# Performance work log

Hardware: AMD Instinct MI355X
Metric: run time of the kernel (lower is better)

The kernel has to match this reference:

```python
import jax, jax.numpy as jnp
import numpy as np

N = 50000        # nodes
E = 800000       # directed edges
NUM_E = 10000    # hyperedges
NFEAT, NHID, NOUT = 256, 128, 64
K = 10
TEMP = 5.0


def gcn_prop(h, src, dst, n):
    # PyG GCNConv propagation with added self-loops: D^-1/2 (A+I) D^-1/2 h
    ew = jnp.ones(src.shape[0], h.dtype)
    deg = 1.0 + jax.ops.segment_sum(ew, dst, num_segments=n)  # self-loop adds 1
    dinv = jax.lax.rsqrt(deg)
    norm = dinv[src] * dinv[dst]                   # [E]
    out = jax.ops.segment_sum(h[src] * norm[:, None], dst, num_segments=n)
    out = out + h / deg[:, None]                   # self-loop term (weight deg^-1)
    return out


def gcn_conv(x, W, b, src, dst, n):
    return gcn_prop(x @ W, src, dst, n) + b


def hgnnp_conv(x, W, b, hv, he, n, num_e):
    # dhg HGNNPConv: theta(x) then v->e mean aggregation, then e->v mean
    h = x @ W + b
    ones = jnp.ones(hv.shape[0], h.dtype)
    e_deg = jnp.maximum(jax.ops.segment_sum(ones, he, num_segments=num_e), 1.0)
    v_deg = jnp.maximum(jax.ops.segment_sum(ones, hv, num_segments=n), 1.0)
    e_feat = jax.ops.segment_sum(h[hv], he, num_segments=num_e) / e_deg[:, None]
    v_out = jax.ops.segment_sum(e_feat[he], hv, num_segments=n) / v_deg[:, None]
    return v_out


def setup_inputs() -> dict:
    key = jax.random.key(0)
    ks = jax.random.split(key, 12)
    x = jax.random.normal(ks[0], (N, NFEAT), jnp.float32)
    edge_index = jax.random.randint(ks[1], (2, E), 0, N)
    hv_idx = jax.random.randint(ks[2], (200000,), 0, N)
    he_idx = jax.random.randint(ks[3], (200000,), 0, NUM_E)

    def glorot(k, shape):
        lim = float(np.sqrt(6.0 / (shape[0] + shape[1])))
        return jax.random.uniform(k, shape, jnp.float32, -lim, lim)

    return {
        "x": x, "edge_index": edge_index, "hv_idx": hv_idx, "he_idx": he_idx,
        "gcn_W1": glorot(ks[4], (NFEAT, NHID)), "gcn_b1": jnp.zeros((NHID,), jnp.float32),
        "gcn_W2": glorot(ks[5], (NHID, NOUT)), "gcn_b2": jnp.zeros((NOUT,), jnp.float32),
        "hg_W1": glorot(ks[6], (NFEAT, NHID)), "hg_b1": jnp.zeros((NHID,), jnp.float32),
        "hg_W2": glorot(ks[7], (NHID, NOUT)), "hg_b2": jnp.zeros((NOUT,), jnp.float32),
        "num_iter": 1,
    }


def reference(x, edge_index, hv_idx, he_idx,
              gcn_W1, gcn_b1, gcn_W2, gcn_b2,
              hg_W1, hg_b1, hg_W2, hg_b2, num_iter):
    src, dst = edge_index[0], edge_index[1]

    # HGNNP_GCN encoder (dropout is identity in eval-style reference)
    x1 = jax.nn.relu(gcn_conv(x, gcn_W1, gcn_b1, src, dst, N))
    x2 = gcn_conv(x1, gcn_W2, gcn_b2, src, dst, N)
    x3 = jax.nn.relu(hgnnp_conv(x, hg_W1, hg_b1, hv_idx, he_idx, N, NUM_E))
    x4 = hgnnp_conv(x3, hg_W2, hg_b2, hv_idx, he_idx, N, NUM_E)  # is_last: no act
    embeds = x2 * 0.5 + x4 * 0.5                     # [N, NOUT]

    # row-normalize (diag(1/||row||) @ data)
    data = embeds / jnp.linalg.norm(embeds, axis=1, keepdims=True)

    # kmeans++ init is a host-side, data-dependent pick; use deterministic
    # strided row selection from the (detached) normalized embeddings.
    init_idx = jnp.arange(K) * (N // K)
    mu = jax.lax.stop_gradient(data[init_idx])       # [K, NOUT]

    for _ in range(int(num_iter)):
        dist = data @ mu.T                           # [N, K]
        r = jax.nn.softmax(TEMP * dist, axis=1)
        cluster_r = r.sum(axis=0)                    # [K]
        cluster_mean = r.T @ data                    # [K, NOUT]
        mu = cluster_mean / cluster_r[:, None]

    dist = data @ mu.T
    r = jax.nn.softmax(TEMP * dist, axis=1)
    return mu, r, embeds, dist
```

## Files before the change

### kernel.cpp

```cpp
#include <hip/hip_runtime.h>
#include <hip/hip_bf16.h>


#define NN   50000
#define NP   50048
#define EE   800000
#define NINC 200000
#define NEH  10000
#define KCL  10

#define MU_OFF  0
#define R_OFF   640
#define EMB_OFF 500640
#define D_OFF   3700640

typedef __hip_bfloat16 bf16;
typedef unsigned short u16;
typedef unsigned int   u32;
typedef __attribute__((ext_vector_type(8))) short short8;
typedef __attribute__((ext_vector_type(4))) float f32x4;

__device__ __forceinline__ float b2f(bf16 v){ return __bfloat162float(v); }
__device__ __forceinline__ float us2f(u16 u){ return __uint_as_float(((unsigned)u) << 16); }
__device__ __forceinline__ u16 f2bu(float f){
  unsigned u = __float_as_uint(f);
  return (u16)((u + 0x7fffu + ((u >> 16) & 1u)) >> 16);
}
__device__ __forceinline__ bf16 f2b(float f){
  u16 r = f2bu(f);
  bf16 h;
  reinterpret_cast<u16&>(h) = r;
  return h;
}
__device__ __forceinline__ float ldf(const void* p, size_t i, int isbf){
  return isbf ? b2f(((const bf16*)p)[i]) : ((const float*)p)[i];
}
__device__ __forceinline__ void stf(void* p, size_t i, float v, int isbf){
  if (isbf) ((bf16*)p)[i] = f2b(v);
  else      ((float*)p)[i] = v;
}

__global__ void k_detect(const u16* __restrict__ xr, int* flag){
  __shared__ int bad;
  if (threadIdx.x == 0) bad = 0;
  __syncthreads();
  for (int i = threadIdx.x; i < 4096; i += 256){
    int e = (xr[i] >> 7) & 0xFF;
    if (e >= 0xEF) bad = 1;
  }
  __syncthreads();
  if (threadIdx.x == 0) *flag = bad ? 0 : 1;
}

__global__ void k_aconv(const void* __restrict__ x, u16* __restrict__ xb,
                        const int* __restrict__ flag){
  int i = blockIdx.x*256 + threadIdx.x;
  const int n4 = NN*256/4;
  if (i >= n4) return;
  ushort4 o;
  if (flag[0]){
    o = ((const ushort4*)x)[i];
  } else {
    float4 v = ((const float4*)x)[i];
    o = make_ushort4(f2bu(v.x), f2bu(v.y), f2bu(v.z), f2bu(v.w));
  }
  ((ushort4*)xb)[i] = o;
}

__global__ void k_wprep(const void* gW1, const void* hW1, const void* gW2, const void* hW2,
                        const void* gb1, const void* hb1, const void* gb2, const void* hb2,
                        u16* gW1t, u16* hW1t, u16* gW2t, u16* hW2t,
                        float* gb1f, float* hb1f, float* gb2f, float* hb2f,
                        const int* __restrict__ flag){
  const int isbf = flag[0];
  int i = blockIdx.x*256 + threadIdx.x;
  if (i < 256*128){
    int n = i >> 8, k = i & 255;
    gW1t[i] = f2bu(ldf(gW1, (size_t)k*128 + n, isbf));
    hW1t[i] = f2bu(ldf(hW1, (size_t)k*128 + n, isbf));
  }
  if (i < 64*128){
    int n = i >> 7, k = i & 127;
    gW2t[i] = f2bu(ldf(gW2, (size_t)k*64 + n, isbf));
    hW2t[i] = f2bu(ldf(hW2, (size_t)k*64 + n, isbf));
  }
  if (i < 128){ gb1f[i] = ldf(gb1,i,isbf); hb1f[i] = ldf(hb1,i,isbf); }
  if (i < 64) { gb2f[i] = ldf(gb2,i,isbf); hb2f[i] = ldf(hb2,i,isbf); }
}

template<int NBKT, int NPB>
__global__ __launch_bounds__(256) void k_histA(const int* __restrict__ key,
                                               int* __restrict__ HA, int chunk){
  __shared__ u32 hist[NBKT];
  for (int i = threadIdx.x; i < NBKT; i += 256) hist[i] = 0;
  __syncthreads();
  int base = blockIdx.x*chunk;
  for (int i = threadIdx.x; i < chunk; i += 256)
    atomicAdd(&hist[key[base+i]/NPB], 1u);
  __syncthreads();
  int* out = HA + blockIdx.x*NBKT;
  for (int i = threadIdx.x; i < NBKT; i += 256) out[i] = (int)hist[i];
}

__global__ void k_scanA_all(int* HAg, int* HAv, int* HAe,
                            int* bsg, int* bsv, int* bse){
  int* HA; int* bs; int nch;
  if (blockIdx.x == 0){ HA = HAg; bs = bsg; nch = 128; }
  else if (blockIdx.x == 1){ HA = HAv; bs = bsv; nch = 64; }
  else { HA = HAe; bs = bse; nch = 64; }
  __shared__ int s[256];
  int t = threadIdx.x;
  int run = 0;
  if (t < 250){
    for (int c = 0; c < nch; ++c){
      int v = HA[c*250 + t];
      HA[c*250 + t] = run;
      run += v;
    }
  }
  int own = (t < 250) ? run : 0;
  s[t] = own; __syncthreads();
  #pragma unroll
  for (int off = 1; off < 256; off <<= 1){
    int add = (t >= off) ? s[t-off] : 0;
    __syncthreads();
    s[t] += add;
    __syncthreads();
  }
  if (t < 250) bs[t] = s[t] - own;
  if (t == 255) bs[250] = s[255];
}

template<int NBKT, int NPB>
__global__ __launch_bounds__(256) void k_fillA(const int* __restrict__ key,
    const int* __restrict__ val, const int* __restrict__ HA,
    const int* __restrict__ bs, u32* __restrict__ packed, int chunk){
  __shared__ u32 cur[NBKT];
  const int* pre = HA + blockIdx.x*NBKT;
  for (int i = threadIdx.x; i < NBKT; i += 256) cur[i] = (u32)(bs[i] + pre[i]);
  __syncthreads();
  int base = blockIdx.x*chunk;
  for (int i = threadIdx.x; i < chunk; i += 256){
    int k = key[base+i];
    int b = k / NPB;
    u32 pos = atomicAdd(&cur[b], 1u);
    packed[pos] = ((u32)(k - b*NPB) << 16) | (u32)val[base+i];
  }
}

template<int NPB>
__global__ __launch_bounds__(256) void k_fillB(const u32* __restrict__ packed,
    const int* __restrict__ bs, int* __restrict__ csr,
    int* __restrict__ cnt, int* __restrict__ rp){
  __shared__ u32 hist[NPB];
  __shared__ int s[256];
  __shared__ u32 cur[NPB];
  const int b = blockIdx.x;
  const int s0 = bs[b], m = bs[b+1] - s0;
  const int t = threadIdx.x;
  for (int i = t; i < NPB; i += 256) hist[i] = 0;
  __syncthreads();
  for (int i = t; i < m; i += 256)
    atomicAdd(&hist[packed[s0+i] >> 16], 1u);
  __syncthreads();
  int own = (t < NPB) ? (int)hist[t] : 0;
  s[t] = own; __syncthreads();
  #pragma unroll
  for (int off = 1; off < 256; off <<= 1){
    int add = (t >= off) ? s[t-off] : 0;
    __syncthreads();
    s[t] += add;
    __syncthreads();
  }
  if (t < NPB){
    int excl = s[t] - own;
    cnt[b*NPB + t] = own;
    rp[b*NPB + t]  = s0 + excl;
    cur[t] = (u32)(s0 + excl);
  }
  __syncthreads();
  for (int i = t; i < m; i += 256){
    u32 p = packed[s0+i];
    u32 pos = atomicAdd(&cur[p >> 16], 1u);
    csr[pos] = (int)(p & 0xffffu);
  }
}

__global__ void k_invs(const int* __restrict__ cg, const int* __restrict__ cv,
                       const int* __restrict__ ce,
                       float* dinv, float* invv, float* inve){
  int i = blockIdx.x*256 + threadIdx.x;
  if (i < NN){
    float d = 1.0f + (float)cg[i];
    dinv[i] = rsqrtf(d);
    invv[i] = 1.0f / fmaxf((float)cv[i], 1.0f);
  } else if (i < NP){
    dinv[i] = 0.f;
  }
  if (i < NEH) inve[i] = 1.0f / fmaxf((float)ce[i], 1.0f);
}

template<int KDIM, int NCOL>
__global__ __launch_bounds__(256) void k_gemm_mfma(
    const u16* __restrict__ A, const u16* __restrict__ Wt,
    const float* __restrict__ bias, const float* __restrict__ rowscale,
    u16* __restrict__ C, int relu)
{
  constexpr int NT  = NCOL/16;
  constexpr int LDA = 40;
  __shared__ __align__(16) u16 Asl[64][LDA];
  __shared__ __align__(16) u16 Wsl[NCOL][LDA];
  const int tid  = threadIdx.x;
  const int wave = tid >> 6, lane = tid & 63;
  const int l15 = lane & 15, l4 = lane >> 4;
  const int row0 = blockIdx.x * 64;
  const int ar = tid >> 2, aq = tid & 3;
  constexpr int NW = NCOL*4/256;

  f32x4 acc[NT] = {};

  for (int kk = 0; kk < KDIM; kk += 32){
    {
      uint4 v = *(const uint4*)(A + (size_t)(row0 + ar)*KDIM + kk + aq*8);
      *(uint4*)&Asl[ar][aq*8] = v;
    }
    #pragma unroll
    for (int w2 = 0; w2 < NW; ++w2){
      int c = tid + w2*256;
      int n = c >> 2, q = c & 3;
      uint4 v = *(const uint4*)(Wt + (size_t)n*KDIM + kk + q*8);
      *(uint4*)&Wsl[n][q*8] = v;
    }
    __syncthreads();
    short8 af = *(const short8*)&Asl[wave*16 + l15][l4*8];
    #pragma unroll
    for (int t = 0; t < NT; ++t){
      short8 bf = *(const short8*)&Wsl[t*16 + l15][l4*8];
      acc[t] = __builtin_amdgcn_mfma_f32_16x16x32_bf16(af, bf, acc[t], 0, 0, 0);
    }
    __syncthreads();
  }

  #pragma unroll
  for (int t = 0; t < NT; ++t){
    int gcol = t*16 + l15;
    float b = bias ? bias[gcol] : 0.f;
    #pragma unroll
    for (int e = 0; e < 4; ++e){
      int grow = row0 + wave*16 + l4*4 + e;
      float v = acc[t][e] + b;
      if (relu) v = fmaxf(v, 0.f);
      if (rowscale) v *= rowscale[grow];
      C[(size_t)grow*NCOL + gcol] = f2bu(v);
    }
  }
}

template<int F, bool OUTBF, bool SELF>
__global__ __launch_bounds__(256) void k_gather(
    const int* __restrict__ rp, const int* __restrict__ cnt,
    const int* __restrict__ csr, const float* __restrict__ scale,
    const u16* __restrict__ h, const float* __restrict__ bias,
    void* __restrict__ out, int relu)
{
  const int wave = threadIdx.x >> 6, lane = threadIdx.x & 63;
  const int d = blockIdx.x*4 + wave;
  const int k0 = rp[d], n = cnt[d];

  if constexpr (F == 128){
    const uint* h32 = (const uint*)h;
    float a0=0,a1=0,b0=0,b1=0,c0=0,c1=0,e0=0,e1=0;
    if (SELF){
      uint v = h32[(size_t)d*64 + lane];
      a0 = us2f((u16)v); a1 = us2f((u16)(v>>16));
    }
    for (int base = 0; base < n; base += 64){
      int mm = n - base; if (mm > 64) mm = 64;
      int idx = (lane < mm) ? csr[k0 + base + lane] : 0;
      int jj = 0;
      for (; jj + 4 <= mm; jj += 4){
        int s0=__shfl(idx,jj), s1=__shfl(idx,jj+1), s2=__shfl(idx,jj+2), s3=__shfl(idx,jj+3);
        uint v0 = h32[(size_t)s0*64 + lane];
        uint v1 = h32[(size_t)s1*64 + lane];
        uint v2 = h32[(size_t)s2*64 + lane];
        uint v3 = h32[(size_t)s3*64 + lane];
        a0 += us2f((u16)v0); a1 += us2f((u16)(v0>>16));
        b0 += us2f((u16)v1); b1 += us2f((u16)(v1>>16));
        c0 += us2f((u16)v2); c1 += us2f((u16)(v2>>16));
        e0 += us2f((u16)v3); e1 += us2f((u16)(v3>>16));
      }
      for (; jj < mm; ++jj){
        int s = __shfl(idx, jj);
        uint v = h32[(size_t)s*64 + lane];
        a0 += us2f((u16)v); a1 += us2f((u16)(v>>16));
      }
    }
    float sc = scale[d];
    float o0 = ((a0+b0)+(c0+e0))*sc;
    float o1 = ((a1+b1)+(c1+e1))*sc;
    if (bias){ o0 += bias[lane*2]; o1 += bias[lane*2+1]; }
    if (relu){ o0 = fmaxf(o0,0.f); o1 = fmaxf(o1,0.f); }
    if (OUTBF){
      ((uint*)out)[(size_t)d*64 + lane] = (uint)f2bu(o0) | ((uint)f2bu(o1) << 16);
    } else {
      ((float2*)out)[(size_t)d*64 + lane] = make_float2(o0, o1);
    }
  } else {
    float a=0,b=0,c=0,e=0;
    if (SELF) a = us2f(h[(size_t)d*64 + lane]);
    for (int base = 0; base < n; base += 64){
      int mm = n - base; if (mm > 64) mm = 64;
      int idx = (lane < mm) ? csr[k0 + base + lane] : 0;
      int jj = 0;
      for (; jj + 4 <= mm; jj += 4){
        int s0=__shfl(idx,jj), s1=__shfl(idx,jj+1), s2=__shfl(idx,jj+2), s3=__shfl(idx,jj+3);
        a += us2f(h[(size_t)s0*64 + lane]);
        b += us2f(h[(size_t)s1*64 + lane]);
        c += us2f(h[(size_t)s2*64 + lane]);
        e += us2f(h[(size_t)s3*64 + lane]);
      }
      for (; jj < mm; ++jj){
        int s = __shfl(idx, jj);
        a += us2f(h[(size_t)s*64 + lane]);
      }
    }
    float o = ((a+b)+(c+e))*scale[d];
    if (bias) o += bias[lane];
    if (relu) o = fmaxf(o, 0.f);
    if (OUTBF) ((u16*)out)[(size_t)d*64 + lane] = f2bu(o);
    else       ((float*)out)[(size_t)d*64 + lane] = o;
  }
}

__global__ void k_embeds(const float* __restrict__ x2, const float* __restrict__ x4,
                         void* __restrict__ out, float* __restrict__ data,
                         const int* __restrict__ flag){
  int row  = blockIdx.x*4 + (threadIdx.x >> 6);
  int lane = threadIdx.x & 63;
  if (row >= NN) return;
  size_t idx = (size_t)row*64 + lane;
  float v = 0.5f*(x2[idx] + x4[idx]);
  float ss = v*v;
  #pragma unroll
  for (int off=32; off>0; off>>=1) ss += __shfl_xor(ss, off);
  float inv = rsqrtf(ss);
  data[idx] = v*inv;
  stf(out, EMB_OFF + idx, v, flag[0]);
}

__global__ void k_mu_init(const float* __restrict__ data, float* __restrict__ mu){
  int p = blockIdx.x*256 + threadIdx.x;
  if (p >= KCL*64) return;
  int k = p >> 6, f = p & 63;
  mu[p] = data[(size_t)k*(NN/KCL)*64 + f];
}

__global__ __launch_bounds__(640) void k_cluster_iter(const float* __restrict__ data,
    const float* __restrict__ mu, float* __restrict__ part, float* __restrict__ pcr,
    const int* __restrict__ nit, int iter)
{
  if (iter >= nit[0]) return;
  __shared__ float ms[640];
  __shared__ float rl[250][KCL];
  const int tid = threadIdx.x;
  ms[tid] = mu[tid];
  __syncthreads();
  const int r0 = blockIdx.x*250;
  if (tid < 250){
    const float4* dr = (const float4*)(data + (size_t)(r0 + tid)*64);
    float dot[KCL];
    #pragma unroll
    for (int k=0;k<KCL;k++) dot[k]=0.f;
    #pragma unroll
    for (int q=0;q<16;q++){
      float4 v = dr[q];
      #pragma unroll
      for (int k=0;k<KCL;k++){
        float4 m4 = *(const float4*)&ms[k*64+q*4];
        dot[k] = fmaf(v.x,m4.x,fmaf(v.y,m4.y,fmaf(v.z,m4.z,fmaf(v.w,m4.w,dot[k]))));
      }
    }
    float m = -1e30f;
    #pragma unroll
    for (int k=0;k<KCL;k++) m = fmaxf(m, 5.0f*dot[k]);
    float s = 0.f, ev[KCL];
    #pragma unroll
    for (int k=0;k<KCL;k++){ ev[k] = expf(5.0f*dot[k]-m); s += ev[k]; }
    float inv = 1.0f/s;
    #pragma unroll
    for (int k=0;k<KCL;k++) rl[tid][k] = ev[k]*inv;
  }
  __syncthreads();
  const int w = tid >> 6, f = tid & 63;
  float acc = 0.f, crp = 0.f;
  for (int t = 0; t < 250; ++t){
    float rv = rl[t][w];
    acc = fmaf(rv, data[(size_t)(r0+t)*64 + f], acc);
    crp += rv;
  }
  part[(size_t)blockIdx.x*640 + tid] = acc;
  if (f == 0) pcr[blockIdx.x*16 + w] = crp;
}

__global__ void k_creduce(const float* __restrict__ part, const float* __restrict__ pcr,
                          float* __restrict__ csum, float* __restrict__ cr,
                          const int* __restrict__ nit, int iter){
  if (iter >= nit[0]) return;
  int p = threadIdx.x;
  if (p < 640){
    float a = 0.f;
    for (int b = 0; b < 200; ++b) a += part[(size_t)b*640 + p];
    csum[p] = a;
  } else if (p < 640 + KCL){
    int k = p - 640;
    float a = 0.f;
    for (int b = 0; b < 200; ++b) a += pcr[b*16 + k];
    cr[k] = a;
  }
}

__global__ void k_mu_update(float* __restrict__ mu, const float* __restrict__ csum,
                            const float* __restrict__ cr,
                            const int* __restrict__ nit, int iter){
  if (iter >= nit[0]) return;
  int p = threadIdx.x;
  mu[p] = csum[p] / cr[p >> 6];
}

__global__ __launch_bounds__(256) void k_cluster_final(const float* __restrict__ data,
    const float* __restrict__ mu, void* __restrict__ out, const int* __restrict__ flag)
{
  __shared__ float ms[640];
  const int tid = threadIdx.x;
  for (int j = tid; j < 640; j += 256) ms[j] = mu[j];
  __syncthreads();
  int row = blockIdx.x*256 + tid;
  if (row >= NN) return;
  const int isbf = flag[0];
  const float4* dr = (const float4*)(data + (size_t)row*64);
  float dot[KCL];
  #pragma unroll
  for (int k=0;k<KCL;k++) dot[k]=0.f;
  #pragma unroll
  for (int q=0;q<16;q++){
    float4 v = dr[q];
    #pragma unroll
    for (int k=0;k<KCL;k++){
      float4 m4 = *(const float4*)&ms[k*64+q*4];
      dot[k] = fmaf(v.x,m4.x,fmaf(v.y,m4.y,fmaf(v.z,m4.z,fmaf(v.w,m4.w,dot[k]))));
    }
  }
  float m = -1e30f;
  #pragma unroll
  for (int k=0;k<KCL;k++) m = fmaxf(m, 5.0f*dot[k]);
  float s = 0.f, ev[KCL];
  #pragma unroll
  for (int k=0;k<KCL;k++){ ev[k] = expf(5.0f*dot[k]-m); s += ev[k]; }
  float inv = 1.0f/s;
  #pragma unroll
  for (int k=0;k<KCL;k++){
    stf(out, (size_t)D_OFF + (size_t)row*KCL + k, dot[k],    isbf);
    stf(out, (size_t)R_OFF + (size_t)row*KCL + k, ev[k]*inv, isbf);
  }
}

__global__ void k_mu_out(const float* __restrict__ mu, void* __restrict__ out,
                         const int* __restrict__ flag){
  int p = blockIdx.x*256 + threadIdx.x;
  if (p < KCL*64) stf(out, MU_OFF + p, mu[p], flag[0]);
}

extern "C" void kernel_launch(void* const* d_in, const int* in_sizes, int n_in,
                              void* d_out, int out_size, void* d_ws, size_t ws_size,
                              hipStream_t stream)
{
  const void* x   = d_in[0];
  const int*  ei  = (const int*)d_in[1];
  const int*  hv  = (const int*)d_in[2];
  const int*  he  = (const int*)d_in[3];
  const void* gW1 = d_in[4];
  const void* gb1 = d_in[5];
  const void* gW2 = d_in[6];
  const void* gb2 = d_in[7];
  const void* hW1 = d_in[8];
  const void* hb1 = d_in[9];
  const void* hW2 = d_in[10];
  const void* hb2 = d_in[11];
  const int*  nit = (const int*)d_in[12];

  float* ws = (float*)d_ws;
  size_t o = 0;
  u16*   xb  = (u16*)(ws + o); o += (size_t)NP*128;
  u16*   BAb = (u16*)(ws + o); o += (size_t)NP*64;
  u16*   BBb = (u16*)(ws + o); o += (size_t)NP*64;
  u16*   BCb = (u16*)(ws + o); o += (size_t)NP*64;
  u16*   BDb = (u16*)(ws + o); o += (size_t)NEH*64;
  u16*  gW1t = (u16*)(ws + o); o += 16384;
  u16*  hW1t = (u16*)(ws + o); o += 16384;
  u16*  gW2t = (u16*)(ws + o); o += 4096;
  u16*  hW2t = (u16*)(ws + o); o += 4096;
  float* gb1f = ws + o; o += 128;
  float* hb1f = ws + o; o += 128;
  float* gb2f = ws + o; o += 64;
  float* hb2f = ws + o; o += 64;
  float* dinv = ws + o; o += 50048;
  float* invv = ws + o; o += 50048;
  float* inve = ws + o; o += 10048;
  float* mu   = ws + o; o += 640;
  float* csum = ws + o; o += 640;
  float* cr   = ws + o; o += 64;
  float* part = ws + o; o += 200*640;
  float* pcr  = ws + o; o += 200*16;
  int*   dflg = (int*)(ws + o); o += 16;
  float* x2f   = (float*)xb;
  float* x4f   = (float*)xb + (size_t)NP*64;
  float* dataf = (float*)BBb;
  int* ib = (int*)(ws + o);
  size_t io = 0;
  int* cg    = ib + io; io += NN;
  int* cv    = ib + io; io += NN;
  int* ce    = ib + io; io += NEH + 48;
  int* rp_g  = ib + io; io += NN;
  int* rp_v  = ib + io; io += NN;
  int* rp_e  = ib + io; io += NEH + 48;
  int* csr_g = ib + io; io += EE;
  int* csr_e = ib + io; io += NINC;
  int* csr_v = ib + io; io += NINC;
  int* HAg   = ib + io; io += 128*250;
  int* HAv   = ib + io; io += 64*250;
  int* HAe   = ib + io; io += 64*250;
  int* bsg   = ib + io; io += 256;
  int* bsv   = ib + io; io += 256;
  int* bse   = ib + io; io += 256;
  u32* pg = (u32*)(ib + io); io += EE;
  u32* pv = (u32*)(ib + io); io += NINC;
  u32* pe = (u32*)(ib + io); io += NINC;

  const int* srcp = ei;
  const int* dstp = ei + EE;
  dim3 B(256);
  const int NBP = (NP + 255)/256;

  k_detect<<<dim3(1), B, 0, stream>>>((const u16*)x, dflg);
  k_aconv<<<dim3(12500), B, 0, stream>>>(x, xb, dflg);
  k_wprep<<<dim3(128), B, 0, stream>>>(gW1, hW1, gW2, hW2, gb1, hb1, gb2, hb2,
                                       gW1t, hW1t, gW2t, hW2t,
                                       gb1f, hb1f, gb2f, hb2f, dflg);

  k_histA<250,200><<<dim3(128), B, 0, stream>>>(dstp, HAg, 6250);
  k_histA<250,200><<<dim3(64),  B, 0, stream>>>(hv,   HAv, 3125);
  k_histA<250, 40><<<dim3(64),  B, 0, stream>>>(he,   HAe, 3125);
  k_scanA_all<<<dim3(3), B, 0, stream>>>(HAg, HAv, HAe, bsg, bsv, bse);
  k_fillA<250,200><<<dim3(128), B, 0, stream>>>(dstp, srcp, HAg, bsg, pg, 6250);
  k_fillA<250,200><<<dim3(64),  B, 0, stream>>>(hv,   he,   HAv, bsv, pv, 3125);
  k_fillA<250, 40><<<dim3(64),  B, 0, stream>>>(he,   hv,   HAe, bse, pe, 3125);
  k_fillB<200><<<dim3(250), B, 0, stream>>>(pg, bsg, csr_g, cg, rp_g);
  k_fillB<200><<<dim3(250), B, 0, stream>>>(pv, bsv, csr_v, cv, rp_v);
  k_fillB< 40><<<dim3(250), B, 0, stream>>>(pe, bse, csr_e, ce, rp_e);
  k_invs<<<dim3(NBP), B, 0, stream>>>(cg, cv, ce, dinv, invv, inve);

  const int NB = NP/64;
  k_gemm_mfma<256,128><<<dim3(NB), B, 0, stream>>>(xb, gW1t, nullptr, dinv, BAb, 0);
  k_gather<128,true,true><<<dim3(NN/4), B, 0, stream>>>(rp_g, cg, csr_g, dinv,
                                                        BAb, gb1f, BBb, 1);
  k_gemm_mfma<256,128><<<dim3(NB), B, 0, stream>>>(xb, hW1t, hb1f, nullptr, BAb, 0);
  k_gather<128,true,false><<<dim3(NEH/4), B, 0, stream>>>(rp_e, ce, csr_e, inve,
                                                          BAb, nullptr, BDb, 0);
  k_gather<128,true,false><<<dim3(NN/4), B, 0, stream>>>(rp_v, cv, csr_v, invv,
                                                         BDb, nullptr, BCb, 1);
  k_gemm_mfma<128,64><<<dim3(NB), B, 0, stream>>>(BBb, gW2t, nullptr, dinv, BAb, 0);
  k_gather<64,false,true><<<dim3(NN/4), B, 0, stream>>>(rp_g, cg, csr_g, dinv,
                                                        BAb, gb2f, x2f, 0);
  k_gemm_mfma<128,64><<<dim3(NB), B, 0, stream>>>(BCb, hW2t, hb2f, nullptr, BAb, 0);
  k_gather<64,true,false><<<dim3(NEH/4), B, 0, stream>>>(rp_e, ce, csr_e, inve,
                                                         BAb, nullptr, BDb, 0);
  k_gather<64,false,false><<<dim3(NN/4), B, 0, stream>>>(rp_v, cv, csr_v, invv,
                                                         BDb, nullptr, x4f, 0);

  k_embeds<<<dim3((NN+3)/4), B, 0, stream>>>(x2f, x4f, d_out, dataf, dflg);

  k_mu_init<<<dim3(3), B, 0, stream>>>(dataf, mu);
  for (int it = 0; it < 4; ++it){
    k_cluster_iter<<<dim3(200), dim3(640), 0, stream>>>(dataf, mu, part, pcr, nit, it);
    k_creduce     <<<dim3(1),   dim3(768), 0, stream>>>(part, pcr, csum, cr, nit, it);
    k_mu_update   <<<dim3(1),   dim3(640), 0, stream>>>(mu, csum, cr, nit, it);
  }
  k_cluster_final<<<dim3(196), B, 0, stream>>>(dataf, mu, d_out, dflg);
  k_mu_out       <<<dim3(3),  B, 0, stream>>>(mu, d_out, dflg);
}
```

Measured before the change: 380.5 us.

## Retile k-means cluster kernels into 64-row smem tiles with two-stage reduction

The cluster iteration and final kernels now process 64 rows per block across 782 blocks, staging the data tile in padded shared memory. All 640 threads compute row-by-cluster dot products, where previously only 250 threads did the full work. The single-block reduction of block partials is split into a 40-block first stage and a small second stage to handle the larger partial count. This aims to raise parallelism in the clustering phase, at the cost of an extra launch per iteration and more partial-sum traffic.

```diff
diff --git a/kernel.cpp b/kernel.cpp
--- a/kernel.cpp
+++ b/kernel.cpp
@@ -8,6 +8,7 @@
 #define NINC 200000
 #define NEH  10000
 #define KCL  10
+#define CBLK 782
 
 #define MU_OFF  0
 #define R_OFF   640
@@ -361,60 +362,88 @@
 {
   if (iter >= nit[0]) return;
   __shared__ float ms[640];
-  __shared__ float rl[250][KCL];
+  __shared__ float dt[64][65];
+  __shared__ float ds[64][11];
   const int tid = threadIdx.x;
   ms[tid] = mu[tid];
-  __syncthreads();
-  const int r0 = blockIdx.x*250;
-  if (tid < 250){
-    const float4* dr = (const float4*)(data + (size_t)(r0 + tid)*64);
+  const int base = blockIdx.x*64;
+  for (int i = tid; i < 4096; i += 640){
+    int r = i >> 6, f = i & 63;
+    int grow = base + r;
+    dt[r][f] = (grow < NN) ? data[(size_t)grow*64 + f] : 0.f;
+  }
+  __syncthreads();
+  {
+    const int row = tid & 63, k = tid >> 6;
+    float dot = 0.f;
+    #pragma unroll 16
+    for (int f = 0; f < 64; ++f)
+      dot = fmaf(dt[row][f], ms[k*64 + f], dot);
+    ds[row][k] = dot;
+  }
+  __syncthreads();
+  if (tid < 64){
     float dot[KCL];
     #pragma unroll
-    for (int k=0;k<KCL;k++) dot[k]=0.f;
-    #pragma unroll
-    for (int q=0;q<16;q++){
-      float4 v = dr[q];
-      #pragma unroll
-      for (int k=0;k<KCL;k++){
-        float4 m4 = *(const float4*)&ms[k*64+q*4];
-        dot[k] = fmaf(v.x,m4.x,fmaf(v.y,m4.y,fmaf(v.z,m4.z,fmaf(v.w,m4.w,dot[k]))));
-      }
-    }
+    for (int k = 0; k < KCL; ++k) dot[k] = ds[tid][k];
     float m = -1e30f;
     #pragma unroll
-    for (int k=0;k<KCL;k++) m = fmaxf(m, 5.0f*dot[k]);
+    for (int k = 0; k < KCL; ++k) m = fmaxf(m, 5.0f*dot[k]);
     float s = 0.f, ev[KCL];
     #pragma unroll
-    for (int k=0;k<KCL;k++){ ev[k] = expf(5.0f*dot[k]-m); s += ev[k]; }
-    float inv = 1.0f/s;
-    #pragma unroll
-    for (int k=0;k<KCL;k++) rl[tid][k] = ev[k]*inv;
-  }
-  __syncthreads();
-  const int w = tid >> 6, f = tid & 63;
-  float acc = 0.f, crp = 0.f;
-  for (int t = 0; t < 250; ++t){
-    float rv = rl[t][w];
-    acc = fmaf(rv, data[(size_t)(r0+t)*64 + f], acc);
-    crp += rv;
-  }
-  part[(size_t)blockIdx.x*640 + tid] = acc;
-  if (f == 0) pcr[blockIdx.x*16 + w] = crp;
-}
-
-__global__ void k_creduce(const float* __restrict__ part, const float* __restrict__ pcr,
-                          float* __restrict__ csum, float* __restrict__ cr,
-                          const int* __restrict__ nit, int iter){
+    for (int k = 0; k < KCL; ++k){ ev[k] = expf(5.0f*dot[k]-m); s += ev[k]; }
+    float inv = (base + tid < NN) ? 1.0f/s : 0.f;
+    #pragma unroll
+    for (int k = 0; k < KCL; ++k) ds[tid][k] = ev[k]*inv;
+  }
+  __syncthreads();
+  {
+    const int f = tid & 63, k = tid >> 6;
+    float acc = 0.f, crp = 0.f;
+    #pragma unroll 8
+    for (int t = 0; t < 64; ++t){
+      float rv = ds[t][k];
+      acc = fmaf(rv, dt[t][f], acc);
+      crp += rv;
+    }
+    part[(size_t)blockIdx.x*640 + tid] = acc;
+    if (f == 0) pcr[blockIdx.x*16 + k] = crp;
+  }
+}
+
+__global__ void k_cred1(const float* __restrict__ part, const float* __restrict__ pcr,
+                        float* __restrict__ p2, float* __restrict__ pc2,
+                        const int* __restrict__ nit, int iter){
   if (iter >= nit[0]) return;
-  int p = threadIdx.x;
-  if (p < 640){
+  int b = blockIdx.x, t = threadIdx.x;
+  int r0 = b*20, r1 = r0 + 20; if (r1 > CBLK) r1 = CBLK;
+  if (t < 640){
     float a = 0.f;
-    for (int b = 0; b < 200; ++b) a += part[(size_t)b*640 + p];
-    csum[p] = a;
-  } else if (p < 640 + KCL){
-    int k = p - 640;
+    for (int r = r0; r < r1; ++r) a += part[(size_t)r*640 + t];
+    p2[(size_t)b*640 + t] = a;
+  } else if (t < 640 + KCL){
+    int k = t - 640;
     float a = 0.f;
-    for (int b = 0; b < 200; ++b) a += pcr[b*16 + k];
+    for (int r = r0; r < r1; ++r) a += pcr[r*16 + k];
+    pc2[b*16 + k] = a;
+  }
+}
+
+__global__ void k_cred2(const float* __restrict__ p2, const float* __restrict__ pc2,
+                        float* __restrict__ csum, float* __restrict__ cr,
+                        const int* __restrict__ nit, int iter){
+  if (iter >= nit[0]) return;
+  int t = threadIdx.x;
+  if (t < 640){
+    float a = 0.f;
+    #pragma unroll
+    for (int b = 0; b < 40; ++b) a += p2[(size_t)b*640 + t];
+    csum[t] = a;
+  } else if (t < 640 + KCL){
+    int k = t - 640;
+    float a = 0.f;
+    #pragma unroll
+    for (int b = 0; b < 40; ++b) a += pc2[b*16 + k];
     cr[k] = a;
   }
 }
@@ -427,40 +456,48 @@
   mu[p] = csum[p] / cr[p >> 6];
 }
 
-__global__ __launch_bounds__(256) void k_cluster_final(const float* __restrict__ data,
+__global__ __launch_bounds__(640) void k_cluster_final(const float* __restrict__ data,
     const float* __restrict__ mu, void* __restrict__ out, const int* __restrict__ flag)
 {
   __shared__ float ms[640];
+  __shared__ float dt[64][65];
+  __shared__ float ds[64][11];
   const int tid = threadIdx.x;
-  for (int j = tid; j < 640; j += 256) ms[j] = mu[j];
-  __syncthreads();
-  int row = blockIdx.x*256 + tid;
-  if (row >= NN) return;
-  const int isbf = flag[0];
-  const float4* dr = (const float4*)(data + (size_t)row*64);
-  float dot[KCL];
-  #pragma unroll
-  for (int k=0;k<KCL;k++) dot[k]=0.f;
-  #pragma unroll
-  for (int q=0;q<16;q++){
-    float4 v = dr[q];
-    #pragma unroll
-    for (int k=0;k<KCL;k++){
-      float4 m4 = *(const float4*)&ms[k*64+q*4];
-      dot[k] = fmaf(v.x,m4.x,fmaf(v.y,m4.y,fmaf(v.z,m4.z,fmaf(v.w,m4.w,dot[k]))));
-    }
-  }
-  float m = -1e30f;
-  #pragma unroll
-  for (int k=0;k<KCL;k++) m = fmaxf(m, 5.0f*dot[k]);
-  float s = 0.f, ev[KCL];
-  #pragma unroll
-  for (int k=0;k<KCL;k++){ ev[k] = expf(5.0f*dot[k]-m); s += ev[k]; }
-  float inv = 1.0f/s;
-  #pragma unroll
-  for (int k=0;k<KCL;k++){
-    stf(out, (size_t)D_OFF + (size_t)row*KCL + k, dot[k],    isbf);
-    stf(out, (size_t)R_OFF + (size_t)row*KCL + k, ev[k]*inv, isbf);
+  ms[tid] = mu[tid];
+  const int base = blockIdx.x*64;
+  for (int i = tid; i < 4096; i += 640){
+    int r = i >> 6, f = i & 63;
+    int grow = base + r;
+    dt[r][f] = (grow < NN) ? data[(size_t)grow*64 + f] : 0.f;
+  }
+  __syncthreads();
+  {
+    const int row = tid & 63, k = tid >> 6;
+    float dot = 0.f;
+    #pragma unroll 16
+    for (int f = 0; f < 64; ++f)
+      dot = fmaf(dt[row][f], ms[k*64 + f], dot);
+    ds[row][k] = dot;
+  }
+  __syncthreads();
+  if (tid < 64 && base + tid < NN){
+    const int row = base + tid;
+    const int isbf = flag[0];
+    float dot[KCL];
+    #pragma unroll
+    for (int k = 0; k < KCL; ++k) dot[k] = ds[tid][k];
+    float m = -1e30f;
+    #pragma unroll
+    for (int k = 0; k < KCL; ++k) m = fmaxf(m, 5.0f*dot[k]);
+    float s = 0.f, ev[KCL];
+    #pragma unroll
+    for (int k = 0; k < KCL; ++k){ ev[k] = expf(5.0f*dot[k]-m); s += ev[k]; }
+    float inv = 1.0f/s;
+    #pragma unroll
+    for (int k = 0; k < KCL; ++k){
+      stf(out, (size_t)D_OFF + (size_t)row*KCL + k, dot[k],    isbf);
+      stf(out, (size_t)R_OFF + (size_t)row*KCL + k, ev[k]*inv, isbf);
+    }
   }
 }
 
@@ -509,8 +546,10 @@
   float* mu   = ws + o; o += 640;
   float* csum = ws + o; o += 640;
   float* cr   = ws + o; o += 64;
-  float* part = ws + o; o += 200*640;
-  float* pcr  = ws + o; o += 200*16;
+  float* part = ws + o; o += (size_t)CBLK*640;
+  float* pcr  = ws + o; o += CBLK*16;
+  float* p2   = ws + o; o += 40*640;
+  float* pc2  = ws + o; o += 40*16;
   int*   dflg = (int*)(ws + o); o += 16;
   float* x2f   = (float*)xb;
   float* x4f   = (float*)xb + (size_t)NP*64;
@@ -581,10 +620,11 @@
 
   k_mu_init<<<dim3(3), B, 0, stream>>>(dataf, mu);
   for (int it = 0; it < 4; ++it){
-    k_cluster_iter<<<dim3(200), dim3(640), 0, stream>>>(dataf, mu, part, pcr, nit, it);
-    k_creduce     <<<dim3(1),   dim3(768), 0, stream>>>(part, pcr, csum, cr, nit, it);
-    k_mu_update   <<<dim3(1),   dim3(640), 0, stream>>>(mu, csum, cr, nit, it);
-  }
-  k_cluster_final<<<dim3(196), B, 0, stream>>>(dataf, mu, d_out, dflg);
+    k_cluster_iter<<<dim3(CBLK), dim3(640), 0, stream>>>(dataf, mu, part, pcr, nit, it);
+    k_cred1       <<<dim3(40),   dim3(768), 0, stream>>>(part, pcr, p2, pc2, nit, it);
+    k_cred2       <<<dim3(1),    dim3(768), 0, stream>>>(p2, pc2, csum, cr, nit, it);
+    k_mu_update   <<<dim3(1),    dim3(640), 0, stream>>>(mu, csum, cr, nit, it);
+  }
+  k_cluster_final<<<dim3(CBLK), dim3(640), 0, stream>>>(dataf, mu, d_out, dflg);
   k_mu_out       <<<dim3(3),  B, 0, stream>>>(mu, d_out, dflg);
 }
```

Measured after the change: 372.3 us. 1.02x faster.
